# Kernel tuning notes

Measured on AMD Instinct MI355X. Metric: run time of the kernel, lower is better.

The kernel has to match this reference:

```python
import jax, jax.numpy as jnp
import numpy as np

MODEL_DIM = 1024
NUM_HEADS = 16
HEAD_DIM = MODEL_DIM // NUM_HEADS
B, SQ, SK = 1, 4096, 4096


def setup_inputs() -> dict:
    key = jax.random.key(0)
    ks = jax.random.split(key, 10)
    s = 0.02  # realistic init scale for weights
    inp = {
        "x_query": jax.random.normal(ks[0], (B, SQ, MODEL_DIM), jnp.float32),
        "x_context": jax.random.normal(ks[1], (B, SK, MODEL_DIM), jnp.float32),
        # causal mask [B,1,Sq,Sk]; 0 -> masked
        "mask": jnp.tril(jnp.ones((SQ, SK), jnp.int32))[None, None, :, :],
        "wq": jax.random.normal(ks[2], (MODEL_DIM, MODEL_DIM), jnp.float32) * s,
        "bq": jnp.zeros((MODEL_DIM,), jnp.float32),
        "wk": jax.random.normal(ks[3], (MODEL_DIM, MODEL_DIM), jnp.float32) * s,
        "bk": jnp.zeros((MODEL_DIM,), jnp.float32),
        "wv": jax.random.normal(ks[4], (MODEL_DIM, MODEL_DIM), jnp.float32) * s,
        "bv": jnp.zeros((MODEL_DIM,), jnp.float32),
        "wo": jax.random.normal(ks[5], (MODEL_DIM, MODEL_DIM), jnp.float32) * s,
        "bo": jnp.zeros((MODEL_DIM,), jnp.float32),
    }
    return inp


def reference(x_query, x_context, mask, wq, bq, wk, bk, wv, bv, wo, bo):
    b = x_query.shape[0]
    # torch nn.Linear: y = x @ W.T + b
    q = x_query @ wq.T + bq
    k = x_context @ wk.T + bk
    v = x_context @ wv.T + bv
    # [B, S, D] -> [B, H, S, Hd]
    def split_heads(t):
        return t.reshape(b, -1, NUM_HEADS, HEAD_DIM).transpose(0, 2, 1, 3)
    q, k, v = split_heads(q), split_heads(k), split_heads(v)
    scale = 1.0 / jnp.sqrt(jnp.asarray(HEAD_DIM, q.dtype))
    scores = jnp.einsum('bhqd,bhkd->bhqk', q, k) * scale  # [B,H,Sq,Sk]
    scores = jnp.where(mask == 0, jnp.asarray(-1e9, scores.dtype), scores)
    attn = jax.nn.softmax(scores, axis=-1)
    # dropout: eval mode (identity)
    ctx = jnp.einsum('bhqk,bhkd->bhqd', attn, v)
    ctx = ctx.transpose(0, 2, 1, 3).reshape(b, -1, MODEL_DIM)
    return ctx @ wo.T + bo
```

## Files before the change

### kernel.cpp

```cpp
#include <hip/hip_runtime.h>

typedef __bf16 bf16x8 __attribute__((ext_vector_type(8)));
typedef float f32x4 __attribute__((ext_vector_type(4)));
typedef float f32x16 __attribute__((ext_vector_type(16)));
typedef unsigned int u32x2v __attribute__((ext_vector_type(2)));

#define GLD16(gp, lp) __builtin_amdgcn_global_load_lds( \
    (const __attribute__((address_space(1))) void*)(gp), \
    (__attribute__((address_space(3))) void*)(lp), 16, 0, 0)

__device__ __forceinline__ unsigned short f2bf(float f) {
  unsigned int u = __float_as_uint(f);
  u += 0x7FFFu + ((u >> 16) & 1u);
  return (unsigned short)(u >> 16);
}

__device__ __forceinline__ unsigned int cvtpk(float lo, float hi) {
  unsigned int r;
  asm("v_cvt_pk_bf16_f32 %0, %1, %2" : "=v"(r) : "v"(lo), "v"(hi));
  return r;
}

__device__ __forceinline__ float exp2f_(float x) {
#if __has_builtin(__builtin_amdgcn_exp2f)
  return __builtin_amdgcn_exp2f(x);
#else
  float r; asm("v_exp_f32 %0, %1" : "=v"(r) : "v"(x)); return r;
#endif
}

__device__ __forceinline__ u32x2v pswap(unsigned int a, unsigned int b) {
#if __has_builtin(__builtin_amdgcn_permlane32_swap)
  u32x2v r;
  auto q = __builtin_amdgcn_permlane32_swap(a, b, false, false);
  r[0] = q[0]; r[1] = q[1];
  return r;
#else
  unsigned int pa = (unsigned int)__shfl_xor((int)a, 32);
  unsigned int pb = (unsigned int)__shfl_xor((int)b, 32);
  int hi = (threadIdx.x >> 5) & 1;
  u32x2v r;
  r[0] = hi ? pb : a;
  r[1] = hi ? b : pa;
  return r;
#endif
}

__global__ __launch_bounds__(256) void cast6(
    const float* __restrict__ xq, const float* __restrict__ xc,
    const float* __restrict__ wq, const float* __restrict__ wk,
    const float* __restrict__ wv, const float* __restrict__ wo,
    unsigned short* __restrict__ d) {
  int i = (blockIdx.x * 256 + threadIdx.x) * 4;
  const float* s; int off;
  if      (i < (4 << 20))  { s = xq; off = 0; }
  else if (i < (8 << 20))  { s = xc; off = 4 << 20; }
  else if (i < (9 << 20))  { s = wq; off = 8 << 20; }
  else if (i < (10 << 20)) { s = wk; off = 9 << 20; }
  else if (i < (11 << 20)) { s = wv; off = 10 << 20; }
  else                     { s = wo; off = 11 << 20; }
  float4 v = *(const float4*)(s + (i - off));
  ushort4 o;
  o.x = f2bf(v.x); o.y = f2bf(v.y); o.z = f2bf(v.z); o.w = f2bf(v.w);
  *(ushort4*)(d + i) = o;
}

template<int OUTF32>
__device__ __forceinline__ void gemm_body(
    const unsigned short* __restrict__ A, const unsigned short* __restrict__ B,
    const float* __restrict__ bias, void* __restrict__ C,
    int N, int K, int bm, int bn, float scale,
    unsigned short* As, unsigned short* Bs) {
  const int t = threadIdx.x;
  const int lane = t & 63, wid = t >> 6;
  const int wm = wid >> 1, wn = wid & 1;
  const int l15 = lane & 15, l4 = lane >> 4, l7 = lane & 7;

  f32x4 acc[4][4];
#pragma unroll
  for (int i = 0; i < 4; ++i)
#pragma unroll
    for (int j = 0; j < 4; ++j) acc[i][j] = (f32x4){0.f, 0.f, 0.f, 0.f};

  const char* Ab = (const char*)A;
  const char* Bb = (const char*)B;
  const int ldb = K * 2;

  for (int kt = 0; kt < K; kt += 64) {
#pragma unroll
    for (int c = 0; c < 4; ++c) {
      int o = c * 4096 + wid * 1024 + lane * 16;
      int row = o >> 7;
      int ch = ((o >> 4) & 7) ^ (row & 7);
      const char* ga = Ab + (size_t)(bm * 128 + row) * ldb + kt * 2 + ch * 16;
      GLD16(ga, (char*)As + c * 4096 + wid * 1024);
      const char* gb = Bb + (size_t)(bn * 128 + row) * ldb + kt * 2 + ch * 16;
      GLD16(gb, (char*)Bs + c * 4096 + wid * 1024);
    }
    __syncthreads();
#pragma unroll
    for (int kk = 0; kk < 2; ++kk) {
      bf16x8 af[4], bfr[4];
#pragma unroll
      for (int mi = 0; mi < 4; ++mi) {
        int row = wm * 64 + mi * 16 + l15;
        int ch = (l4 + 4 * kk) ^ l7;
        af[mi] = *(const bf16x8*)((const char*)As + row * 128 + ch * 16);
      }
#pragma unroll
      for (int ni = 0; ni < 4; ++ni) {
        int row = wn * 64 + ni * 16 + l15;
        int ch = (l4 + 4 * kk) ^ l7;
        bfr[ni] = *(const bf16x8*)((const char*)Bs + row * 128 + ch * 16);
      }
#pragma unroll
      for (int mi = 0; mi < 4; ++mi)
#pragma unroll
        for (int ni = 0; ni < 4; ++ni)
          acc[mi][ni] = __builtin_amdgcn_mfma_f32_16x16x32_bf16(
              af[mi], bfr[ni], acc[mi][ni], 0, 0, 0);
    }
    __syncthreads();
  }

#pragma unroll
  for (int ni = 0; ni < 4; ++ni) {
    int col = bn * 128 + wn * 64 + ni * 16 + l15;
    float bv = bias[col];
#pragma unroll
    for (int mi = 0; mi < 4; ++mi) {
#pragma unroll
      for (int r = 0; r < 4; ++r) {
        int row = bm * 128 + wm * 64 + mi * 16 + l4 * 4 + r;
        float v = (acc[mi][ni][r] + bv) * scale;
        if (OUTF32) ((float*)C)[(size_t)row * N + col] = v;
        else ((unsigned short*)C)[(size_t)row * N + col] = f2bf(v);
      }
    }
  }
}

__global__ __launch_bounds__(256) void gemm_qkv(
    const unsigned short* __restrict__ xq, const unsigned short* __restrict__ xc,
    const unsigned short* __restrict__ wq, const unsigned short* __restrict__ wk,
    const unsigned short* __restrict__ wv,
    const float* __restrict__ bq, const float* __restrict__ bk,
    const float* __restrict__ bv,
    unsigned short* __restrict__ Qo, unsigned short* __restrict__ Ko,
    unsigned short* __restrict__ Vo) {
  __shared__ __align__(16) unsigned short As[128 * 64];
  __shared__ __align__(16) unsigned short Bs[128 * 64];
  const unsigned short* A; const unsigned short* B; const float* bias;
  unsigned short* C; float scale;
  if (blockIdx.z == 0)      { A = xq; B = wq; bias = bq; C = Qo; scale = 0.18033688011112042f; }
  else if (blockIdx.z == 1) { A = xc; B = wk; bias = bk; C = Ko; scale = 1.0f; }
  else                      { A = xc; B = wv; bias = bv; C = Vo; scale = 1.0f; }
  gemm_body<0>(A, B, bias, (void*)C, 1024, 1024, blockIdx.y, blockIdx.x, scale, As, Bs);
}

__global__ __launch_bounds__(256) void gemm_out(
    const unsigned short* __restrict__ A, const unsigned short* __restrict__ B,
    const float* __restrict__ bias, float* __restrict__ C) {
  __shared__ __align__(16) unsigned short As[128 * 64];
  __shared__ __align__(16) unsigned short Bs[128 * 64];
  gemm_body<1>(A, B, bias, (void*)C, 1024, 1024, blockIdx.y, blockIdx.x, 1.0f, As, Bs);
}

__global__ __launch_bounds__(256)
void flash_attn(
    const unsigned short* __restrict__ Q, const unsigned short* __restrict__ K,
    const unsigned short* __restrict__ V, unsigned short* __restrict__ O,
    unsigned short* __restrict__ partO, float* __restrict__ lBase) {
  __shared__ __align__(16) char smem[32768];

  const int b = blockIdx.x;
  const int h = b & 15;
  const int ep = b >> 4;
  int qb, role, P;
  if (ep < 30)      { qb = 31 - ep / 3; role = ep % 3; P = 3; }
  else if (ep < 52) { int k = ep - 30; qb = 21 - (k >> 1); role = k & 1; P = 2; }
  else              { qb = 10 - (ep - 52); role = 0; P = 1; }

  const int T = 2 * qb + 2;
  const int t0 = (role * T) / P;
  const int n  = ((role + 1) * T) / P - t0;

  const int t = threadIdx.x;
  const int lane = t & 63, w = t >> 6;
  const int l31 = lane & 31, hi = lane >> 5;
  const int q0w = qb * 128 + w * 32;
  const int qwmax = q0w + 31;

  bf16x8 qf[4];
#pragma unroll
  for (int ks = 0; ks < 4; ++ks)
    qf[ks] = *(const bf16x8*)(Q + (size_t)(q0w + l31) * 1024 + h * 64 + ks * 16 + hi * 8);

  f32x16 po0, po1;
#pragma unroll
  for (int r = 0; r < 16; ++r) { po0[r] = 0.f; po1[r] = 0.f; }
  float lacc[8];
#pragma unroll
  for (int i = 0; i < 8; ++i) lacc[i] = 0.f;

  const int vd4 = (t & 15) * 4;
  const int vkvr = (t >> 4) * 4;
  uint2 va[4];

  auto stageK = [&](int tile, int buf) {
#pragma unroll
    for (int i = 0; i < 2; ++i) {
      int id = i * 256 + t;
      int row = id >> 3;
      int ch = (id & 7) ^ (row & 7);
      GLD16((const char*)K + (size_t)(tile * 64 + row) * 2048 + h * 128 + ch * 16,
            smem + buf * 8192 + id * 16);
    }
  };
  auto loadV = [&](int tile) {
#pragma unroll
    for (int i = 0; i < 4; ++i)
      va[i] = *(const uint2*)(V + (size_t)(tile * 64 + vkvr + i) * 1024 + h * 64 + vd4);
  };
  auto writeV = [&](int buf) {
    char* Vt = smem + 16384 + buf * 8192;
#pragma unroll
    for (int j = 0; j < 4; ++j) {
      unsigned sel = (j & 1) ? 0x07060302u : 0x05040100u;
      unsigned s01 = (j < 2) ? __builtin_amdgcn_perm(va[1].x, va[0].x, sel)
                             : __builtin_amdgcn_perm(va[1].y, va[0].y, sel);
      unsigned s23 = (j < 2) ? __builtin_amdgcn_perm(va[3].x, va[2].x, sel)
                             : __builtin_amdgcn_perm(va[3].y, va[2].y, sel);
      int row = vd4 + j;
      int sw = (vkvr * 2) ^ (((row >> 2) & 7) << 4);
      *(uint2*)(Vt + row * 128 + sw) = make_uint2(s01, s23);
    }
  };

  stageK(t0, 0);
  loadV(t0);
  writeV(0);
  __syncthreads();

  for (int it = 0; it < n; ++it) {
    const int c = it & 1;
    const bool pf = (it + 1) < n;
    if (pf) { stageK(t0 + it + 1, c ^ 1); loadV(t0 + it + 1); }

    const int kv0 = (t0 + it) * 64;
    if (kv0 <= qwmax) {
      const char* Ks = smem + c * 8192;
      const char* Vt = smem + 16384 + c * 8192;
      f32x16 s0, s1;
#pragma unroll
      for (int r = 0; r < 16; ++r) { s0[r] = 0.f; s1[r] = 0.f; }
      __builtin_amdgcn_s_setprio(1);
#pragma unroll
      for (int ks = 0; ks < 4; ++ks) {
        int c0 = ((ks * 2 + hi) ^ (l31 & 7)) << 4;
        bf16x8 k0 = *(const bf16x8*)(Ks + l31 * 128 + c0);
        bf16x8 k1 = *(const bf16x8*)(Ks + (32 + l31) * 128 + c0);
        s0 = __builtin_amdgcn_mfma_f32_32x32x16_bf16(k0, qf[ks], s0, 0, 0, 0);
        s1 = __builtin_amdgcn_mfma_f32_32x32x16_bf16(k1, qf[ks], s1, 0, 0, 0);
      }
      __builtin_amdgcn_s_setprio(0);
      if (kv0 + 63 > q0w) {
        int q = q0w + l31;
#pragma unroll
        for (int r = 0; r < 16; ++r) {
          int kvi = kv0 + (r & 3) + 8 * (r >> 2) + 4 * hi;
          if (kvi > q) s0[r] = -1e30f;
          if (kvi + 32 > q) s1[r] = -1e30f;
        }
      }
#pragma unroll
      for (int r = 0; r < 16; ++r) s0[r] = exp2f_(s0[r]);
#pragma unroll
      for (int r = 0; r < 16; ++r) s1[r] = exp2f_(s1[r]);
#pragma unroll
      for (int i = 0; i < 8; ++i)
        lacc[i] += (s0[2 * i] + s0[2 * i + 1]) + (s1[2 * i] + s1[2 * i + 1]);

#pragma unroll
      for (int kp = 0; kp < 4; ++kp) {
        const f32x16& sv = (kp < 2) ? s0 : s1;
        const int bb = (kp & 1) * 8;
        unsigned c0v = cvtpk(sv[bb + 0], sv[bb + 1]);
        unsigned c1v = cvtpk(sv[bb + 2], sv[bb + 3]);
        unsigned c2v = cvtpk(sv[bb + 4], sv[bb + 5]);
        unsigned c3v = cvtpk(sv[bb + 6], sv[bb + 7]);
        u32x2v w02 = pswap(c0v, c2v);
        u32x2v w13 = pswap(c1v, c3v);
        union { unsigned u[4]; bf16x8 v; } pfr;
        pfr.u[0] = w02[0]; pfr.u[1] = w13[0]; pfr.u[2] = w02[1]; pfr.u[3] = w13[1];
        int cb = kp * 2 + hi;
        __builtin_amdgcn_s_setprio(1);
        {
          int row = l31;
          bf16x8 vf = *(const bf16x8*)(Vt + row * 128 + ((cb ^ ((row >> 2) & 7)) << 4));
          po0 = __builtin_amdgcn_mfma_f32_32x32x16_bf16(vf, pfr.v, po0, 0, 0, 0);
        }
        {
          int row = 32 + l31;
          bf16x8 vf = *(const bf16x8*)(Vt + row * 128 + ((cb ^ ((row >> 2) & 7)) << 4));
          po1 = __builtin_amdgcn_mfma_f32_32x32x16_bf16(vf, pfr.v, po1, 0, 0, 0);
        }
        __builtin_amdgcn_s_setprio(0);
      }
    }
    if (pf) writeV(c ^ 1);
    __syncthreads();
  }

  float l4[4];
#pragma unroll
  for (int i = 0; i < 4; ++i) l4[i] = lacc[i] + lacc[4 + i];
  float ps = (l4[0] + l4[1]) + (l4[2] + l4[3]);
  u32x2v sw2 = pswap(__float_as_uint(ps), __float_as_uint(ps));
  const float l_i = __uint_as_float(sw2[0]) + __uint_as_float(sw2[1]);
  const float rinv = 1.0f / l_i;

  if (P > 1) {
    const int slot = h * 52 + ep;
    unsigned u[16];
#pragma unroll
    for (int i = 0; i < 8; ++i) u[i] = cvtpk(po0[2 * i] * rinv, po0[2 * i + 1] * rinv);
#pragma unroll
    for (int i = 0; i < 8; ++i) u[8 + i] = cvtpk(po1[2 * i] * rinv, po1[2 * i + 1] * rinv);
    char* bO = (char*)partO + (size_t)slot * 16384 + t * 64;
    *(uint4*)(bO +  0) = make_uint4(u[0], u[1], u[2], u[3]);
    *(uint4*)(bO + 16) = make_uint4(u[4], u[5], u[6], u[7]);
    *(uint4*)(bO + 32) = make_uint4(u[8], u[9], u[10], u[11]);
    *(uint4*)(bO + 48) = make_uint4(u[12], u[13], u[14], u[15]);
    if (!hi) {
      lBase[(size_t)slot * 128 + w * 32 + l31] = l_i;
    }
    return;
  }

  {
    int qlocal = w * 32 + l31;
#pragma unroll
    for (int g = 0; g < 4; ++g) {
#pragma unroll
      for (int db = 0; db < 2; ++db) {
        const f32x16& p = db ? po1 : po0;
        unsigned w0 = cvtpk(p[g * 4 + 0] * rinv, p[g * 4 + 1] * rinv);
        unsigned w1 = cvtpk(p[g * 4 + 2] * rinv, p[g * 4 + 3] * rinv);
        int d0 = db * 32 + 8 * g + 4 * hi;
        int byte = qlocal * 128 + ((d0 * 2) ^ ((qlocal & 7) << 4));
        *(uint2*)(smem + byte) = make_uint2(w0, w1);
      }
    }
  }
  __syncthreads();
#pragma unroll
  for (int it = 0; it < 4; ++it) {
    int r = it * 32 + (t >> 3);
    int c = t & 7;
    uint4 val = *(const uint4*)(smem + r * 128 + ((c ^ (r & 7)) << 4));
    *(uint4*)((char*)O + (size_t)(qb * 128 + r) * 2048 + h * 128 + c * 16) = val;
  }
}

__global__ __launch_bounds__(256) void flash_merge(
    const unsigned short* __restrict__ partO, const float* __restrict__ lBase,
    unsigned short* __restrict__ O) {
  const int p = blockIdx.x;
  const int h = p & 15;
  const int j = p >> 4;
  int qb, P, e0;
  if (j < 10) { qb = 31 - j; P = 3; e0 = j * 3; }
  else        { qb = 21 - (j - 10); P = 2; e0 = 30 + (j - 10) * 2; }
  const int t = threadIdx.x;
  const int s = t >> 6, hi = (t >> 5) & 1, l31 = t & 31;

  float acc[32];
#pragma unroll
  for (int i = 0; i < 32; ++i) acc[i] = 0.f;
  float den = 0.f;
#pragma unroll
  for (int r = 0; r < 3; ++r) {
    if (r < P) {
      float wgt = lBase[(size_t)(h * 52 + e0 + r) * 128 + s * 32 + l31];
      den += wgt;
      const uint4* bO = (const uint4*)((const char*)partO +
                         (size_t)(h * 52 + e0 + r) * 16384 + t * 64);
      uint4 a = bO[0], b2 = bO[1], c2 = bO[2], d2 = bO[3];
      unsigned uu[16] = {a.x, a.y, a.z, a.w, b2.x, b2.y, b2.z, b2.w,
                         c2.x, c2.y, c2.z, c2.w, d2.x, d2.y, d2.z, d2.w};
#pragma unroll
      for (int i = 0; i < 16; ++i) {
        acc[2 * i]     += wgt * __uint_as_float(uu[i] << 16);
        acc[2 * i + 1] += wgt * __uint_as_float(uu[i] & 0xFFFF0000u);
      }
    }
  }
  float rinv = 1.0f / den;
  const int q = qb * 128 + s * 32 + l31;
  unsigned short* orow = O + (size_t)q * 1024 + h * 64;
#pragma unroll
  for (int r = 0; r < 16; ++r) {
    int d = (r & 3) + 8 * (r >> 2) + 4 * hi;
    orow[d]      = f2bf(acc[r] * rinv);
    orow[d + 32] = f2bf(acc[16 + r] * rinv);
  }
}

extern "C" void kernel_launch(void* const* d_in, const int* in_sizes, int n_in,
                              void* d_out, int out_size, void* d_ws, size_t ws_size,
                              hipStream_t stream) {
  const float* xq = (const float*)d_in[0];
  const float* xc = (const float*)d_in[1];
  const float* wq = (const float*)d_in[3];
  const float* bq = (const float*)d_in[4];
  const float* wk = (const float*)d_in[5];
  const float* bk = (const float*)d_in[6];
  const float* wv = (const float*)d_in[7];
  const float* bv = (const float*)d_in[8];
  const float* wo = (const float*)d_in[9];
  const float* bo = (const float*)d_in[10];

  unsigned short* wsb = (unsigned short*)d_ws;
  unsigned short* xqb = wsb;
  unsigned short* xcb = wsb + (4 << 20);
  unsigned short* wqb = wsb + (8 << 20);
  unsigned short* wkb = wsb + (9 << 20);
  unsigned short* wvb = wsb + (10 << 20);
  unsigned short* wob = wsb + (11 << 20);
  unsigned short* Qb  = wsb + (12 << 20);
  unsigned short* Kb  = wsb + (16 << 20);
  unsigned short* Vb  = wsb + (20 << 20);
  unsigned short* Cb  = wsb + (24 << 20);

  unsigned short* partO = (unsigned short*)d_ws;
  float* lBase = (float*)((char*)d_ws + (14u << 20));

  cast6<<<12288, 256, 0, stream>>>(xq, xc, wq, wk, wv, wo, wsb);

  dim3 gq(1024 / 128, 4096 / 128, 3);
  gemm_qkv<<<gq, 256, 0, stream>>>(xqb, xcb, wqb, wkb, wvb, bq, bk, bv, Qb, Kb, Vb);

  flash_attn<<<1008, 256, 0, stream>>>(Qb, Kb, Vb, Cb, partO, lBase);

  flash_merge<<<336, 256, 0, stream>>>(partO, lBase, Cb);

  dim3 go(1024 / 128, 4096 / 128);
  gemm_out<<<go, 256, 0, stream>>>(Cb, wob, bo, (float*)d_out);
}
```

Baseline: 156.0 us.

## Widen GEMM blocks to 8 waves and rebalance attention split-K partitions

The projection GEMMs now run 512-thread blocks. Each wave computes a 32x64 sub-tile instead of 64x64, which halves accumulator registers per wave and doubles waves per tile. Flash attention splits the longest causal query blocks into up to 4 KV partitions, with 4/3/2/1 tiers, giving 1280 blocks and 384 merge blocks to even out per-block work. The V tile is single-buffered with an added barrier to cut shared memory and raise occupancy, at the cost of losing overlap between V writes and compute, more merge traffic, and more partial-output workspace.

```diff
diff --git a/kernel.cpp b/kernel.cpp
--- a/kernel.cpp
+++ b/kernel.cpp
@@ -76,9 +76,9 @@
   const int wm = wid >> 1, wn = wid & 1;
   const int l15 = lane & 15, l4 = lane >> 4, l7 = lane & 7;
 
-  f32x4 acc[4][4];
-#pragma unroll
-  for (int i = 0; i < 4; ++i)
+  f32x4 acc[2][4];
+#pragma unroll
+  for (int i = 0; i < 2; ++i)
 #pragma unroll
     for (int j = 0; j < 4; ++j) acc[i][j] = (f32x4){0.f, 0.f, 0.f, 0.f};
 
@@ -88,22 +88,22 @@
 
   for (int kt = 0; kt < K; kt += 64) {
 #pragma unroll
-    for (int c = 0; c < 4; ++c) {
-      int o = c * 4096 + wid * 1024 + lane * 16;
-      int row = o >> 7;
-      int ch = ((o >> 4) & 7) ^ (row & 7);
+    for (int c = 0; c < 2; ++c) {
+      int id = c * 512 + t;
+      int row = id >> 3;
+      int ch = (id & 7) ^ (row & 7);
       const char* ga = Ab + (size_t)(bm * 128 + row) * ldb + kt * 2 + ch * 16;
-      GLD16(ga, (char*)As + c * 4096 + wid * 1024);
+      GLD16(ga, (char*)As + id * 16);
       const char* gb = Bb + (size_t)(bn * 128 + row) * ldb + kt * 2 + ch * 16;
-      GLD16(gb, (char*)Bs + c * 4096 + wid * 1024);
+      GLD16(gb, (char*)Bs + id * 16);
     }
     __syncthreads();
 #pragma unroll
     for (int kk = 0; kk < 2; ++kk) {
-      bf16x8 af[4], bfr[4];
-#pragma unroll
-      for (int mi = 0; mi < 4; ++mi) {
-        int row = wm * 64 + mi * 16 + l15;
+      bf16x8 af[2], bfr[4];
+#pragma unroll
+      for (int mi = 0; mi < 2; ++mi) {
+        int row = wm * 32 + mi * 16 + l15;
         int ch = (l4 + 4 * kk) ^ l7;
         af[mi] = *(const bf16x8*)((const char*)As + row * 128 + ch * 16);
       }
@@ -114,7 +114,7 @@
         bfr[ni] = *(const bf16x8*)((const char*)Bs + row * 128 + ch * 16);
       }
 #pragma unroll
-      for (int mi = 0; mi < 4; ++mi)
+      for (int mi = 0; mi < 2; ++mi)
 #pragma unroll
         for (int ni = 0; ni < 4; ++ni)
           acc[mi][ni] = __builtin_amdgcn_mfma_f32_16x16x32_bf16(
@@ -128,10 +128,10 @@
     int col = bn * 128 + wn * 64 + ni * 16 + l15;
     float bv = bias[col];
 #pragma unroll
-    for (int mi = 0; mi < 4; ++mi) {
+    for (int mi = 0; mi < 2; ++mi) {
 #pragma unroll
       for (int r = 0; r < 4; ++r) {
-        int row = bm * 128 + wm * 64 + mi * 16 + l4 * 4 + r;
+        int row = bm * 128 + wm * 32 + mi * 16 + l4 * 4 + r;
         float v = (acc[mi][ni][r] + bv) * scale;
         if (OUTF32) ((float*)C)[(size_t)row * N + col] = v;
         else ((unsigned short*)C)[(size_t)row * N + col] = f2bf(v);
@@ -140,7 +140,7 @@
   }
 }
 
-__global__ __launch_bounds__(256) void gemm_qkv(
+__global__ __launch_bounds__(512) void gemm_qkv(
     const unsigned short* __restrict__ xq, const unsigned short* __restrict__ xc,
     const unsigned short* __restrict__ wq, const unsigned short* __restrict__ wk,
     const unsigned short* __restrict__ wv,
@@ -158,7 +158,7 @@
   gemm_body<0>(A, B, bias, (void*)C, 1024, 1024, blockIdx.y, blockIdx.x, scale, As, Bs);
 }
 
-__global__ __launch_bounds__(256) void gemm_out(
+__global__ __launch_bounds__(512) void gemm_out(
     const unsigned short* __restrict__ A, const unsigned short* __restrict__ B,
     const float* __restrict__ bias, float* __restrict__ C) {
   __shared__ __align__(16) unsigned short As[128 * 64];
@@ -171,15 +171,16 @@
     const unsigned short* __restrict__ Q, const unsigned short* __restrict__ K,
     const unsigned short* __restrict__ V, unsigned short* __restrict__ O,
     unsigned short* __restrict__ partO, float* __restrict__ lBase) {
-  __shared__ __align__(16) char smem[32768];
+  __shared__ __align__(16) char smem[24576];
 
   const int b = blockIdx.x;
   const int h = b & 15;
   const int ep = b >> 4;
   int qb, role, P;
-  if (ep < 30)      { qb = 31 - ep / 3; role = ep % 3; P = 3; }
-  else if (ep < 52) { int k = ep - 30; qb = 21 - (k >> 1); role = k & 1; P = 2; }
-  else              { qb = 10 - (ep - 52); role = 0; P = 1; }
+  if (ep < 32)      { qb = 31 - (ep >> 2); role = ep & 3; P = 4; }
+  else if (ep < 56) { int k = ep - 32; qb = 23 - k / 3; role = k % 3; P = 3; }
+  else if (ep < 72) { int k = ep - 56; qb = 15 - (k >> 1); role = k & 1; P = 2; }
+  else              { qb = 7 - (ep - 72); role = 0; P = 1; }
 
   const int T = 2 * qb + 2;
   const int t0 = (role * T) / P;
@@ -222,8 +223,8 @@
     for (int i = 0; i < 4; ++i)
       va[i] = *(const uint2*)(V + (size_t)(tile * 64 + vkvr + i) * 1024 + h * 64 + vd4);
   };
-  auto writeV = [&](int buf) {
-    char* Vt = smem + 16384 + buf * 8192;
+  auto writeV = [&]() {
+    char* Vt = smem + 16384;
 #pragma unroll
     for (int j = 0; j < 4; ++j) {
       unsigned sel = (j & 1) ? 0x07060302u : 0x05040100u;
@@ -239,7 +240,7 @@
 
   stageK(t0, 0);
   loadV(t0);
-  writeV(0);
+  writeV();
   __syncthreads();
 
   for (int it = 0; it < n; ++it) {
@@ -250,7 +251,7 @@
     const int kv0 = (t0 + it) * 64;
     if (kv0 <= qwmax) {
       const char* Ks = smem + c * 8192;
-      const char* Vt = smem + 16384 + c * 8192;
+      const char* Vt = smem + 16384;
       f32x16 s0, s1;
 #pragma unroll
       for (int r = 0; r < 16; ++r) { s0[r] = 0.f; s1[r] = 0.f; }
@@ -308,20 +309,21 @@
         __builtin_amdgcn_s_setprio(0);
       }
     }
-    if (pf) writeV(c ^ 1);
     __syncthreads();
-  }
-
-  float l4[4];
-#pragma unroll
-  for (int i = 0; i < 4; ++i) l4[i] = lacc[i] + lacc[4 + i];
-  float ps = (l4[0] + l4[1]) + (l4[2] + l4[3]);
+    if (pf) writeV();
+    __syncthreads();
+  }
+
+  float l4v[4];
+#pragma unroll
+  for (int i = 0; i < 4; ++i) l4v[i] = lacc[i] + lacc[4 + i];
+  float ps = (l4v[0] + l4v[1]) + (l4v[2] + l4v[3]);
   u32x2v sw2 = pswap(__float_as_uint(ps), __float_as_uint(ps));
   const float l_i = __uint_as_float(sw2[0]) + __uint_as_float(sw2[1]);
   const float rinv = 1.0f / l_i;
 
   if (P > 1) {
-    const int slot = h * 52 + ep;
+    const int slot = h * 72 + ep;
     unsigned u[16];
 #pragma unroll
     for (int i = 0; i < 8; ++i) u[i] = cvtpk(po0[2 * i] * rinv, po0[2 * i + 1] * rinv);
@@ -370,8 +372,9 @@
   const int h = p & 15;
   const int j = p >> 4;
   int qb, P, e0;
-  if (j < 10) { qb = 31 - j; P = 3; e0 = j * 3; }
-  else        { qb = 21 - (j - 10); P = 2; e0 = 30 + (j - 10) * 2; }
+  if (j < 8)       { qb = 31 - j; P = 4; e0 = j * 4; }
+  else if (j < 16) { qb = 23 - (j - 8); P = 3; e0 = 32 + (j - 8) * 3; }
+  else             { qb = 15 - (j - 16); P = 2; e0 = 56 + (j - 16) * 2; }
   const int t = threadIdx.x;
   const int s = t >> 6, hi = (t >> 5) & 1, l31 = t & 31;
 
@@ -380,12 +383,12 @@
   for (int i = 0; i < 32; ++i) acc[i] = 0.f;
   float den = 0.f;
 #pragma unroll
-  for (int r = 0; r < 3; ++r) {
+  for (int r = 0; r < 4; ++r) {
     if (r < P) {
-      float wgt = lBase[(size_t)(h * 52 + e0 + r) * 128 + s * 32 + l31];
+      float wgt = lBase[(size_t)(h * 72 + e0 + r) * 128 + s * 32 + l31];
       den += wgt;
       const uint4* bO = (const uint4*)((const char*)partO +
-                         (size_t)(h * 52 + e0 + r) * 16384 + t * 64);
+                         (size_t)(h * 72 + e0 + r) * 16384 + t * 64);
       uint4 a = bO[0], b2 = bO[1], c2 = bO[2], d2 = bO[3];
       unsigned uu[16] = {a.x, a.y, a.z, a.w, b2.x, b2.y, b2.z, b2.w,
                          c2.x, c2.y, c2.z, c2.w, d2.x, d2.y, d2.z, d2.w};
@@ -434,17 +437,17 @@
   unsigned short* Cb  = wsb + (24 << 20);
 
   unsigned short* partO = (unsigned short*)d_ws;
-  float* lBase = (float*)((char*)d_ws + (14u << 20));
+  float* lBase = (float*)((char*)d_ws + (18u << 20));
 
   cast6<<<12288, 256, 0, stream>>>(xq, xc, wq, wk, wv, wo, wsb);
 
   dim3 gq(1024 / 128, 4096 / 128, 3);
-  gemm_qkv<<<gq, 256, 0, stream>>>(xqb, xcb, wqb, wkb, wvb, bq, bk, bv, Qb, Kb, Vb);
-
-  flash_attn<<<1008, 256, 0, stream>>>(Qb, Kb, Vb, Cb, partO, lBase);
-
-  flash_merge<<<336, 256, 0, stream>>>(partO, lBase, Cb);
+  gemm_qkv<<<gq, 512, 0, stream>>>(xqb, xcb, wqb, wkb, wvb, bq, bk, bv, Qb, Kb, Vb);
+
+  flash_attn<<<1280, 256, 0, stream>>>(Qb, Kb, Vb, Cb, partO, lBase);
+
+  flash_merge<<<384, 256, 0, stream>>>(partO, lBase, Cb);
 
   dim3 go(1024 / 128, 4096 / 128);
-  gemm_out<<<go, 256, 0, stream>>>(Cb, wob, bo, (float*)d_out);
-}
+  gemm_out<<<go, 512, 0, stream>>>(Cb, wob, bo, (float*)d_out);
+}
```

Result: faster. 152.9 us (-2.0%).
